# Performance work log

Measured on AMD Instinct MI355X. Metric: run time of the kernel, lower is better.

## Reference

```python
import jax, jax.numpy as jnp
import numpy as np

ND, NPR, DD, DP, LAT, AT, B = 2048, 2048, 128, 128, 128, 32, 16384


def setup_inputs():
    key = jax.random.key(0)
    ks = jax.random.split(key, 20)
    s = 0.05
    d = {}
    d["e_p_adj"] = (jax.random.uniform(ks[0], (ND, NPR)) < 0.05).astype(jnp.float32)
    d["e_e_adj"] = (jax.random.uniform(ks[1], (ND, ND)) < 0.05).astype(jnp.float32)
    d["p_p_adj"] = (jax.random.uniform(ks[2], (NPR, NPR)) < 0.05).astype(jnp.float32)
    d["input_disease"] = jax.random.randint(ks[3], (B,), 0, ND)
    d["input_drug"] = jax.random.randint(ks[4], (B,), 0, NPR)
    d["labels"] = jax.random.randint(ks[5], (B,), 0, 2)
    # learned parameters
    d["disease_emb"] = jax.random.normal(ks[6], (ND, DD)) * s
    d["drug_emb"] = jax.random.normal(ks[7], (NPR, DP)) * s
    d["Wdg"] = jax.random.normal(ks[8], (DP, LAT)) * s   # disease_gcn_w
    d["bdg_lin"] = jnp.zeros((LAT,))                      # Linear bias
    d["bdg"] = jnp.zeros((LAT,))                          # extra disease_gcn_b
    d["Wpg"] = jax.random.normal(ks[9], (DD, LAT)) * s   # drug_gcn_w
    d["bpg_lin"] = jnp.zeros((LAT,))
    d["bpg"] = jnp.zeros((LAT,))
    d["Wa1_d"] = jax.random.normal(ks[10], (DP + DD, AT)) * s  # concat [key(drug), query(disease)]
    d["ba1_d"] = jnp.zeros((AT,))
    d["Wa2_d"] = jax.random.normal(ks[11], (AT, 1)) * s
    d["ba2_d"] = jnp.zeros((1,))
    d["Wa1_p"] = jax.random.normal(ks[12], (DD + DP, AT)) * s  # concat [key(disease), query(drug)]
    d["ba1_p"] = jnp.zeros((AT,))
    d["Wa2_p"] = jax.random.normal(ks[13], (AT, 1)) * s
    d["ba2_p"] = jnp.zeros((1,))
    d["Wd2"] = jax.random.normal(ks[14], (DD, LAT)) * s  # disease_w2
    d["bd2"] = jnp.zeros((LAT,))
    d["Wp3"] = jax.random.normal(ks[15], (DP, LAT)) * s  # drug_w3
    d["bp3"] = jnp.zeros((LAT,))
    d["mlp_W1"] = jax.random.normal(ks[16], (LAT, DD)) * s
    d["mlp_b1"] = jnp.zeros((DD,))
    d["mlp_W2"] = jax.random.normal(ks[17], (DD, DD)) * s
    d["mlp_b2"] = jnp.zeros((DD,))
    d["Wpred"] = jax.random.normal(ks[18], (DD, 1)) * s
    d["bpred"] = jnp.zeros((1,))
    return d


def _attention_gcn(adj, other, selfe, W1, b1, W2, b2):
    # torch: concat([key=other, query=self]) -> Linear(W1) ; split W1 instead of
    # materializing the [Ns, No, Dk+Dq] concat tensor (same math, less HBM traffic)
    do = other.shape[1]
    ko = other @ W1[:do]              # [No, A]
    qs = selfe @ W1[do:]              # [Ns, A]
    h = jax.nn.relu(qs[:, None, :] + ko[None, :, :] + b1)   # [Ns, No, A]
    alpha = jax.nn.relu(jnp.squeeze(h @ W2, -1) + b2[0])    # [Ns, No]
    alpha = alpha * adj
    return jax.nn.softmax(alpha, axis=1) @ other            # [Ns, Do]


def _forward(e_p_adj, e_e_adj, p_p_adj, input_disease, input_drug, labels,
             disease_emb, drug_emb, Wdg, bdg_lin, bdg, Wpg, bpg_lin, bpg,
             Wa1_d, ba1_d, Wa2_d, ba2_d, Wa1_p, ba1_p, Wa2_p, ba2_p,
             Wd2, bd2, Wp3, bp3, mlp_W1, mlp_b1, mlp_W2, mlp_b2, Wpred, bpred):
    h_e_gcn = _attention_gcn(e_p_adj, drug_emb, disease_emb, Wa1_d, ba1_d, Wa2_d, ba2_d)
    h_e_gcn = h_e_gcn @ Wdg + bdg_lin + bdg
    h_p_gcn = _attention_gcn(e_p_adj.T, disease_emb, drug_emb, Wa1_p, ba1_p, Wa2_p, ba2_p)
    h_p_gcn = h_p_gcn @ Wpg + bpg_lin + bpg
    # disease knn branch
    deg_d = jnp.sum(e_e_adj, axis=1, keepdims=True) + 1e-8
    h_e_e = ((e_e_adj @ disease_emb) / deg_d) @ Wd2 + bd2
    h_e = jax.nn.selu(h_e_gcn + h_e_e)
    # drug knn branch
    deg_p = jnp.sum(p_p_adj, axis=1, keepdims=True) + 1e-8
    h_p_p = ((p_p_adj @ drug_emb) / deg_p) @ Wp3 + bp3
    h_p = jax.nn.selu(h_p_gcn + h_p_p)
    # pair prediction MLP
    x = h_e[input_disease] * h_p[input_drug]                # [B, LAT]
    x = jax.nn.selu(x @ mlp_W1 + mlp_b1)
    x = jax.nn.selu(x @ mlp_W2 + mlp_b2)
    z = jnp.squeeze(x @ Wpred, -1) + bpred[0]               # [B]
    y = labels.astype(jnp.float32)
    # BCEWithLogitsLoss (stable), mean reduction
    loss = jnp.mean(jnp.maximum(z, 0.0) - z * y + jnp.log1p(jnp.exp(-jnp.abs(z))))
    return (loss, jax.nn.sigmoid(z))


def reference(e_p_adj, e_e_adj, p_p_adj, input_disease, input_drug, labels,
              disease_emb, drug_emb, Wdg, bdg_lin, bdg, Wpg, bpg_lin, bpg,
              Wa1_d, ba1_d, Wa2_d, ba2_d, Wa1_p, ba1_p, Wa2_p, ba2_p,
              Wd2, bd2, Wp3, bp3, mlp_W1, mlp_b1, mlp_W2, mlp_b2, Wpred, bpred):
    return _forward(e_p_adj, e_e_adj, p_p_adj, input_disease, input_drug, labels,
                    disease_emb, drug_emb, Wdg, bdg_lin, bdg, Wpg, bpg_lin, bpg,
                    Wa1_d, ba1_d, Wa2_d, ba2_d, Wa1_p, ba1_p, Wa2_p, ba2_p,
                    Wd2, bd2, Wp3, bp3, mlp_W1, mlp_b1, mlp_W2, mlp_b2, Wpred, bpred)
```

## Files before the change

### kernel.cpp

```cpp
#include <hip/hip_runtime.h>

#define ND   2048
#define BB   16384

typedef unsigned short u16;
typedef unsigned int u32;
typedef __attribute__((ext_vector_type(8))) short short8;
typedef __attribute__((ext_vector_type(4))) float f32x4;

__device__ inline float bf2f(u16 u) {
    union { u32 i; float f; } v; v.i = ((u32)u) << 16; return v.f;
}
__device__ inline u16 f2bf(float f) {
    union { float f; u32 i; } v; v.f = f;
    u32 i = v.i + 0x7fffu + ((v.i >> 16) & 1u);
    return (u16)(i >> 16);
}
__device__ inline float seluf(float x) {
    const float sc = 1.0507009873554805f, al = 1.6732632423543772f;
    return x > 0.f ? sc * x : sc * al * expm1f(x);
}

__device__ inline bool sniff_f32(const void* demb_raw, void* lds) {
    int tid = threadIdx.x;
    int* redf = (int*)lds;
    const u16* p6 = (const u16*)demb_raw;
    int sane = 0;
    #pragma unroll
    for (int i = 0; i < 2; i++) {
        u16 u = p6[4 * tid + 2 * i];
        int e = (u >> 7) & 0xFF;
        if (u == 0 || (e >= 0x66 && e <= 0x8C)) sane++;
    }
    redf[tid] = sane;
    __syncthreads();
    for (int o = 128; o > 0; o >>= 1) {
        if (tid < o) redf[tid] += redf[tid + o];
        __syncthreads();
    }
    bool f32 = redf[0] < 300;
    __syncthreads();
    return f32;
}

#define NSEG 26
struct CvtArgs { const void* src[NSEG]; int off[NSEG]; int n[NSEG]; };
struct CS {
    const void* adj[3];
    u16* ridx[3]; u32* rcnt[3];
    const void* demb_raw;
    u32* cntT; float* lossacc; u32* losscnt;
};

__global__ __launch_bounds__(256) void cvtcsr(CvtArgs a, u16* __restrict__ base, CS c) {
    int bx = blockIdx.x;
    int t = threadIdx.x;
    __shared__ int sniffbuf[256];
    bool f32 = sniff_f32(c.demb_raw, sniffbuf);
    if (bx < 8) c.cntT[bx * 256 + t] = 0u;
    if (bx == 8 && t == 0) { c.lossacc[0] = 0.f; c.losscnt[0] = 0u; }
    if (bx < 1536) {
        int m = bx >> 9;
        int r0 = (bx & 511) * 4;
        int lane = t & 63;
        __shared__ u32 lcnt[4];
        if (t < 4) lcnt[t] = 0;
        __syncthreads();
        float v[4][8];
        int c0 = t * 8;
        if (f32) {
            #pragma unroll
            for (int rr = 0; rr < 4; rr++) {
                const float4* p = (const float4*)((const float*)c.adj[m] +
                                                  (size_t)(r0 + rr) * 2048 + c0);
                float4 x = p[0], y = p[1];
                v[rr][0] = x.x; v[rr][1] = x.y; v[rr][2] = x.z; v[rr][3] = x.w;
                v[rr][4] = y.x; v[rr][5] = y.y; v[rr][6] = y.z; v[rr][7] = y.w;
            }
        } else {
            #pragma unroll
            for (int rr = 0; rr < 4; rr++) {
                const uint4* p = (const uint4*)((const u16*)c.adj[m] +
                                                (size_t)(r0 + rr) * 2048 + c0);
                uint4 x = p[0];
                u32 u[4] = {x.x, x.y, x.z, x.w};
                #pragma unroll
                for (int i = 0; i < 4; i++) {
                    v[rr][2 * i + 0] = (u[i] & 0xffffu) ? 1.f : 0.f;
                    v[rr][2 * i + 1] = (u[i] >> 16)     ? 1.f : 0.f;
                }
            }
        }
        #pragma unroll
        for (int rr = 0; rr < 4; rr++) {
            int cnt = 0;
            #pragma unroll
            for (int i = 0; i < 8; i++) cnt += (v[rr][i] != 0.f) ? 1 : 0;
            int pfx = cnt;
            #pragma unroll
            for (int o = 1; o < 64; o <<= 1) {
                int s = __shfl_up(pfx, o, 64);
                if (lane >= o) pfx += s;
            }
            int wtot = __shfl(pfx, 63, 64);
            u32 wb = 0;
            if (lane == 0) wb = atomicAdd(&lcnt[rr], (u32)wtot);
            wb = __shfl((int)wb, 0, 64);
            int o = (int)wb + pfx - cnt;
            u16* ridx = c.ridx[m] + (size_t)(r0 + rr) * 2048;
            #pragma unroll
            for (int i = 0; i < 8; i++) {
                if (v[rr][i] != 0.f) ridx[o++] = (u16)(c0 + i);
            }
        }
        __syncthreads();
        if (t < 4) c.rcnt[m][r0 + t] = lcnt[t];
    } else {
        int idx = bx - 1536;
        int seg = idx >> 6, xb = idx & 63;
        int n = a.n[seg];
        const void* s = a.src[seg];
        u16* d = base + a.off[seg];
        int nw = n >> 1;
        if (f32) {
            const float2* sf = (const float2*)s;
            u32* dw = (u32*)d;
            for (int i = xb * 256 + t; i < nw; i += 16384) {
                float2 v = sf[i];
                dw[i] = (u32)f2bf(v.x) | ((u32)f2bf(v.y) << 16);
            }
        } else {
            const u32* sw = (const u32*)s;
            u32* dw = (u32*)d;
            for (int i = xb * 256 + t; i < nw; i += 16384) dw[i] = sw[i];
        }
        if ((n & 1) && xb == 0 && t == 0)
            d[n - 1] = f32 ? f2bf(((const float*)s)[n - 1]) : ((const u16*)s)[n - 1];
    }
}

struct PR {
    const u16* demb; const u16* pemb;
    const u16* Wa1d; const u16* ba1d;
    const u16* Wa1p; const u16* ba1p;
    float* ko_d; float* qs_d; float* ko_p; float* qs_p;
    const u16* idx0; const u32* cnt0; u16* cidx; u32* ccnt;
    const u16* ts[6]; u16* W1T; u16* W2T; u16* WcTe; u16* WcTp;
    const u16* ba[3]; const u16* bb[3]; u16* b_e; u16* b_p;
    float* csd; float* csp;
    const u16* avgidx[2]; const u32* avgcnt[2]; const u16* avgemb[2]; u16* avgout[2];
};

__global__ __launch_bounds__(256) void prep2(PR p) {
    int bx = blockIdx.x;
    int tid = threadIdx.x;
    __shared__ float sx[2][128];
    __shared__ float sred[2][128];
    __shared__ u16 stile[32][33];
    __shared__ float st0[256], st1[256];
    __shared__ u16 Wl[4096];

    if (bx < 4) {
        int id = bx;
        int m = id >> 1, half = id & 1;
        const u16* e = m ? p.pemb : p.demb;
        int c2 = tid & 31, rg = tid >> 5;
        int dbase = half * 64;
        float s0 = 0.f, s1 = 0.f;
        for (int it = 0; it < 256; it++) {
            int row = it * 8 + rg;
            u32 v = *(const u32*)(e + (size_t)row * 128 + dbase + c2 * 2);
            s0 += bf2f((u16)(v & 0xffffu));
            s1 += bf2f((u16)(v >> 16));
        }
        st0[tid] = s0; st1[tid] = s1;
        __syncthreads();
        if (tid < 32) {
            float a0 = 0.f, a1 = 0.f;
            #pragma unroll
            for (int g = 0; g < 8; g++) { a0 += st0[g * 32 + tid]; a1 += st1[g * 32 + tid]; }
            float* cs = m ? p.csp : p.csd;
            cs[dbase + tid * 2 + 0] = a0;
            cs[dbase + tid * 2 + 1] = a1;
        }
        if (tid < 64) {
            int d = dbase + tid;
            if (m == 0)
                p.b_e[d] = f2bf(bf2f(p.ba[0][d]) + bf2f(p.ba[1][d]) + bf2f(p.ba[2][d]));
            else
                p.b_p[d] = f2bf(bf2f(p.bb[0][d]) + bf2f(p.bb[1][d]) + bf2f(p.bb[2][d]));
        }
    } else if (bx < 2052) {
        int r = bx - 4;
        int n = (int)p.cnt0[r];
        const u16* row = p.idx0 + (size_t)r * 2048;
        for (int i = tid; i < n; i += 256) {
            int cc = (int)row[i];
            u32 q = atomicAdd(&p.ccnt[cc], 1u);
            p.cidx[(size_t)cc * 2048 + q] = (u16)r;
        }
    } else if (bx < 3076) {
        int id = bx - 2052;
        int task = id >> 9, blk = id & 511;
        int wv = tid >> 6, lane = tid & 63;
        int grp = lane >> 4, dim = lane & 15;
        int r = blk * 4 + wv;
        const u16* idx = p.avgidx[task] + (size_t)r * 2048;
        int nnz = (int)p.avgcnt[task][r];
        const u16* emb = p.avgemb[task];
        float acc[8];
        #pragma unroll
        for (int t = 0; t < 8; t++) acc[t] = 0.f;
        for (int base = 0; base < nnz; base += 64) {
            int i = base + lane;
            int j = (i < nnz) ? (int)idx[i] : 0;
            int cend = min(64, nnz - base);
            #pragma unroll 4
            for (int k4 = 0; k4 < cend; k4 += 4) {
                int kk = k4 + grp;
                int jk = __shfl(j, kk, 64);
                float wk = (base + kk < nnz) ? 1.f : 0.f;
                const uint4* pp = (const uint4*)((const char*)emb + jk * 256 + dim * 16);
                uint4 vv = *pp;
                u32 u[4] = {vv.x, vv.y, vv.z, vv.w};
                #pragma unroll
                for (int cc = 0; cc < 4; cc++) {
                    acc[2 * cc + 0] = fmaf(wk, bf2f((u16)(u[cc] & 0xffffu)), acc[2 * cc + 0]);
                    acc[2 * cc + 1] = fmaf(wk, bf2f((u16)(u[cc] >> 16)), acc[2 * cc + 1]);
                }
            }
        }
        #pragma unroll
        for (int t = 0; t < 8; t++) {
            acc[t] += __shfl_xor(acc[t], 32, 64);
            acc[t] += __shfl_xor(acc[t], 16, 64);
        }
        if (grp == 0) {
            float sc = 1.f / ((float)nnz + 1e-8f);
            float v[8];
            #pragma unroll
            for (int t = 0; t < 8; t++) v[t] = acc[t] * sc;
            uint4 pk;
            pk.x = (u32)f2bf(v[0]) | ((u32)f2bf(v[1]) << 16);
            pk.y = (u32)f2bf(v[2]) | ((u32)f2bf(v[3]) << 16);
            pk.z = (u32)f2bf(v[4]) | ((u32)f2bf(v[5]) << 16);
            pk.w = (u32)f2bf(v[6]) | ((u32)f2bf(v[7]) << 16);
            *(uint4*)(p.avgout[task] + (size_t)r * 256 + dim * 8) = pk;
        }
    } else if (bx < 4100) {
        int blk = bx - 3076;
        int m = blk >> 8;
        int r0 = (blk & 255) * 8;
        const u16* src; const u16* W; const u16* bias; float* out;
        switch (m) {
            case 0:  src = p.pemb; W = p.Wa1d;            bias = nullptr; out = p.ko_d; break;
            case 1:  src = p.demb; W = p.Wa1d + 128 * 32; bias = p.ba1d;  out = p.qs_d; break;
            case 2:  src = p.demb; W = p.Wa1p;            bias = nullptr; out = p.ko_p; break;
            default: src = p.pemb; W = p.Wa1p + 128 * 32; bias = p.ba1p;  out = p.qs_p; break;
        }
        {
            const uint4* wsrc = (const uint4*)W;
            uint4* wdst = (uint4*)Wl;
            #pragma unroll
            for (int i = 0; i < 2; i++) wdst[i * 256 + tid] = wsrc[i * 256 + tid];
        }
        __syncthreads();
        int sub = tid >> 7, t = tid & 127;
        int a = t & 31, part = t >> 5;
        #pragma unroll 1
        for (int rp = 0; rp < 4; rp++) {
            int row = r0 + rp * 2 + sub;
            sx[sub][t] = bf2f(src[(size_t)row * 128 + t]);
            __syncthreads();
            float s = 0.f;
            #pragma unroll
            for (int k = 0; k < 32; k++)
                s += sx[sub][part * 32 + k] * bf2f(Wl[(part * 32 + k) * 32 + a]);
            sred[sub][t] = s;
            __syncthreads();
            if (part == 0) {
                float tt = sred[sub][a] + sred[sub][a + 32] + sred[sub][a + 64] + sred[sub][a + 96];
                if (bias) tt += bf2f(bias[a]);
                out[(size_t)row * 32 + a] = tt;
            }
            __syncthreads();
        }
    } else {
        int id = bx - 4100;
        int z = id >> 4, rem = id & 15;
        int c0 = (rem & 3) * 32, r0 = (rem >> 2) * 32;
        const u16* in = p.ts[z];
        u16* out; int ldo, ooff;
        switch (z) {
            case 0:  out = p.W1T;  ldo = 128; ooff = 0;   break;
            case 1:  out = p.W2T;  ldo = 128; ooff = 0;   break;
            case 2:  out = p.WcTe; ldo = 256; ooff = 0;   break;
            case 3:  out = p.WcTe; ldo = 256; ooff = 128; break;
            case 4:  out = p.WcTp; ldo = 256; ooff = 0;   break;
            default: out = p.WcTp; ldo = 256; ooff = 128; break;
        }
        int tx = tid & 31, ty = tid >> 5;
        int x = c0 + tx;
        for (int i = ty; i < 32; i += 8)
            stile[i][tx] = in[(size_t)(r0 + i) * 128 + x];
        __syncthreads();
        int rr = r0 + tx;
        for (int i = ty; i < 32; i += 8)
            out[(size_t)(c0 + i) * ldo + ooff + rr] = stile[tx][i];
    }
}

struct SP {
    const u16* idx[2]; const u32* cnt[2];
    const float* ko[2]; const float* qs[2];
    const u16* w2[2]; const u16* b2[2];
    const u16* emb[2]; const float* csum[2];
    u16* out[2];
};

__global__ __launch_bounds__(256) void spagg(SP a) {
    int task = blockIdx.y;
    int tid = threadIdx.x;
    int wv = tid >> 6, lane = tid & 63;
    int grp = lane >> 4, dim = lane & 15;
    int r = blockIdx.x * 4 + wv;
    const u16* idx = a.idx[task] + (size_t)r * 2048;
    int nnz = (int)a.cnt[task][r];
    const u16* emb = a.emb[task];
    const float* ko = a.ko[task];

    float qsr[32], w2h[32];
    {
        const float4* qp = (const float4*)(a.qs[task] + (size_t)r * 32);
        #pragma unroll
        for (int i = 0; i < 8; i++) {
            float4 v = qp[i];
            qsr[4 * i + 0] = v.x; qsr[4 * i + 1] = v.y;
            qsr[4 * i + 2] = v.z; qsr[4 * i + 3] = v.w;
        }
        #pragma unroll
        for (int i = 0; i < 32; i++) w2h[i] = bf2f(a.w2[task][i]);
    }
    float b2v = bf2f(a.b2[task][0]);

    float acc[8];
    #pragma unroll
    for (int t = 0; t < 8; t++) acc[t] = 0.f;
    float wsuml = 0.f;

    for (int base = 0; base < nnz; base += 64) {
        int i = base + lane;
        float w = 0.f;
        int j = 0;
        if (i < nnz) {
            j = (int)idx[i];
            const float4* kp = (const float4*)(ko + (size_t)j * 32);
            float s = 0.f;
            #pragma unroll
            for (int q = 0; q < 8; q++) {
                float4 kv = kp[q];
                s += fmaxf(qsr[4 * q + 0] + kv.x, 0.f) * w2h[4 * q + 0];
                s += fmaxf(qsr[4 * q + 1] + kv.y, 0.f) * w2h[4 * q + 1];
                s += fmaxf(qsr[4 * q + 2] + kv.z, 0.f) * w2h[4 * q + 2];
                s += fmaxf(qsr[4 * q + 3] + kv.w, 0.f) * w2h[4 * q + 3];
            }
            w = __expf(fmaxf(s + b2v, 0.f)) - 1.f;
            wsuml += w;
        }
        int cend = min(64, nnz - base);
        #pragma unroll 4
        for (int k4 = 0; k4 < cend; k4 += 4) {
            int kk = k4 + grp;
            float wk = __shfl(w, kk, 64);
            int jk = __shfl(j, kk, 64);
            const uint4* pp = (const uint4*)((const char*)emb + jk * 256 + dim * 16);
            uint4 vv = *pp;
            u32 u[4] = {vv.x, vv.y, vv.z, vv.w};
            #pragma unroll
            for (int cc = 0; cc < 4; cc++) {
                acc[2 * cc + 0] = fmaf(wk, bf2f((u16)(u[cc] & 0xffffu)), acc[2 * cc + 0]);
                acc[2 * cc + 1] = fmaf(wk, bf2f((u16)(u[cc] >> 16)), acc[2 * cc + 1]);
            }
        }
    }

    #pragma unroll
    for (int t = 0; t < 8; t++) {
        acc[t] += __shfl_xor(acc[t], 32, 64);
        acc[t] += __shfl_xor(acc[t], 16, 64);
    }
    #pragma unroll
    for (int o = 32; o > 0; o >>= 1) wsuml += __shfl_xor(wsuml, o, 64);

    if (grp == 0) {
        float sc = 1.f / (2048.f + wsuml);
        const float* cs = a.csum[task] + dim * 8;
        float v[8];
        #pragma unroll
        for (int t = 0; t < 8; t++) v[t] = (cs[t] + acc[t]) * sc;
        uint4 pk;
        pk.x = (u32)f2bf(v[0]) | ((u32)f2bf(v[1]) << 16);
        pk.y = (u32)f2bf(v[2]) | ((u32)f2bf(v[3]) << 16);
        pk.z = (u32)f2bf(v[4]) | ((u32)f2bf(v[5]) << 16);
        pk.w = (u32)f2bf(v[6]) | ((u32)f2bf(v[7]) << 16);
        *(uint4*)(a.out[task] + (size_t)r * 256 + dim * 8) = pk;
    }
}

struct GD4 {
    const void* A[4]; const u16* BT[4]; u16* C[4];
    const u16* bias[4]; const float* rs[4];
    int lda[4], ldb[4], ldc[4], coff[4], kiters[4], act[4], araw[4], rsmode[4];
};

#define PADK 136

__global__ __launch_bounds__(256, 2) void gemmL(GD4 g) {
    __shared__ __align__(16) u16 As[16][PADK];
    __shared__ __align__(16) u16 Bs[128][PADK];
    int z = blockIdx.y;
    const void* A = g.A[z];
    const u16* BT = g.BT[z];
    int lda = g.lda[z], ldb = g.ldb[z];
    int kiters = g.kiters[z];
    int tid = threadIdx.x;
    int lane = tid & 63, wv = tid >> 6;
    int mrow = lane & 15, quad = lane >> 4;
    int m0 = blockIdx.x * 16;
    int c0 = wv * 32;
    int sr = tid >> 4, sk = (tid & 15) * 8;
    f32x4 acc0 = {0.f, 0.f, 0.f, 0.f}, acc1 = {0.f, 0.f, 0.f, 0.f};

    short8 ra, rb[8];
    auto ldstage = [&](int kb) {
        ra = *(const short8*)((const u16*)A + (size_t)(m0 + sr) * lda + kb + sk);
        const u16* bbase = BT + (size_t)sr * ldb + kb + sk;
        #pragma unroll
        for (int i = 0; i < 8; i++)
            rb[i] = *(const short8*)(bbase + (size_t)i * 16 * ldb);
    };
    auto ststage = [&]() {
        *(short8*)(&As[sr][sk]) = ra;
        #pragma unroll
        for (int i = 0; i < 8; i++)
            *(short8*)(&Bs[i * 16 + sr][sk]) = rb[i];
    };
    auto compute = [&]() {
        #pragma unroll
        for (int ks = 0; ks < 4; ks++) {
            short8 af = *(const short8*)(&As[mrow][ks * 32 + quad * 8]);
            short8 b0 = *(const short8*)(&Bs[c0 + mrow][ks * 32 + quad * 8]);
            short8 b1 = *(const short8*)(&Bs[c0 + 16 + mrow][ks * 32 + quad * 8]);
            acc0 = __builtin_amdgcn_mfma_f32_16x16x32_bf16(af, b0, acc0, 0, 0, 0);
            acc1 = __builtin_amdgcn_mfma_f32_16x16x32_bf16(af, b1, acc1, 0, 0, 0);
        }
    };

    ldstage(0);
    #pragma unroll 1
    for (int it = 0; it < kiters - 1; ++it) {
        ststage();
        __syncthreads();
        ldstage((it + 1) * 128);
        compute();
        __syncthreads();
    }
    ststage();
    __syncthreads();
    compute();

    const float* rs = g.rs[z];
    int rsmode = g.rsmode[z];
    const u16* bi = g.bias[z];
    u16* C = g.C[z];
    int ldc = g.ldc[z], coff = g.coff[z], act = g.act[z];
    int n0 = c0 + mrow, n1 = n0 + 16;
    float bv0 = bi ? bf2f(bi[n0]) : 0.f;
    float bv1 = bi ? bf2f(bi[n1]) : 0.f;
    #pragma unroll
    for (int r = 0; r < 4; r++) {
        int row = m0 + quad * 4 + r;
        float v0 = acc0[r], v1 = acc1[r];
        if (rsmode == 1) { float sc = rs[row]; v0 *= sc; v1 *= sc; }
        else if (rsmode == 2) {
            float t = 0.f;
            #pragma unroll
            for (int p = 0; p < 8; p++) t += rs[row + p * 2048];
            float sc = 1.f / t;
            v0 *= sc; v1 *= sc;
        }
        v0 += bv0; v1 += bv1;
        if (act) { v0 = seluf(v0); v1 = seluf(v1); }
        C[(size_t)row * ldc + coff + n0] = f2bf(v0);
        C[(size_t)row * ldc + coff + n1] = f2bf(v1);
    }
}

#define PADX 136
__global__ __launch_bounds__(256, 2) void mlpfused(
    const u16* __restrict__ he, const u16* __restrict__ hp,
    const int* __restrict__ di, const int* __restrict__ dr,
    const u16* __restrict__ W1T, const u16* __restrict__ b1,
    const u16* __restrict__ W2T, const u16* __restrict__ b2,
    const u16* __restrict__ wpred, const u16* __restrict__ bpred,
    const int* __restrict__ labels,
    float* __restrict__ out, float* __restrict__ lossacc,
    u32* __restrict__ losscnt) {
    __shared__ __align__(16) u16 Xs[64][PADX];
    __shared__ __align__(16) u16 Ws[128][PADX];
    __shared__ float wred[4];
    int tid = threadIdx.x;
    int lane = tid & 63, wv = tid >> 6;
    int mrow = lane & 15, quad = lane >> 4;
    int p0 = blockIdx.x * 64;

    {
        int row = tid >> 2, sub = tid & 3;
        int b = p0 + row;
        int ia = di[b], ic = dr[b];
        const uint4* pe = (const uint4*)(he + (size_t)ia * 128 + sub * 32);
        const uint4* pp = (const uint4*)(hp + (size_t)ic * 128 + sub * 32);
        #pragma unroll
        for (int q = 0; q < 4; q++) {
            uint4 ue = pe[q], up = pp[q];
            u32 eu[4] = {ue.x, ue.y, ue.z, ue.w};
            u32 pu[4] = {up.x, up.y, up.z, up.w};
            #pragma unroll
            for (int c = 0; c < 4; c++) {
                float lo = bf2f((u16)(eu[c] & 0xffffu)) * bf2f((u16)(pu[c] & 0xffffu));
                float hi = bf2f((u16)(eu[c] >> 16)) * bf2f((u16)(pu[c] >> 16));
                *(u32*)(&Xs[row][sub * 32 + q * 8 + c * 2]) =
                    (u32)f2bf(lo) | ((u32)f2bf(hi) << 16);
            }
        }
    }
    {
        int n = tid >> 1, half = tid & 1;
        const short8* src = (const short8*)(W1T + (size_t)n * 128 + half * 64);
        short8* dst = (short8*)(&Ws[n][half * 64]);
        #pragma unroll
        for (int i = 0; i < 8; i++) dst[i] = src[i];
    }
    __syncthreads();

    f32x4 acc[8];
    #pragma unroll
    for (int nt = 0; nt < 8; nt++) acc[nt] = {0.f, 0.f, 0.f, 0.f};
    #pragma unroll
    for (int ks = 0; ks < 4; ks++) {
        short8 af = *(const short8*)(&Xs[wv * 16 + mrow][ks * 32 + quad * 8]);
        #pragma unroll
        for (int nt = 0; nt < 8; nt++) {
            short8 bfv = *(const short8*)(&Ws[nt * 16 + mrow][ks * 32 + quad * 8]);
            acc[nt] = __builtin_amdgcn_mfma_f32_16x16x32_bf16(af, bfv, acc[nt], 0, 0, 0);
        }
    }
    __syncthreads();
    #pragma unroll
    for (int nt = 0; nt < 8; nt++) {
        int col = nt * 16 + mrow;
        float bv = bf2f(b1[col]);
        #pragma unroll
        for (int r = 0; r < 4; r++) {
            int row = wv * 16 + quad * 4 + r;
            Xs[row][col] = f2bf(seluf(acc[nt][r] + bv));
        }
    }
    {
        int n = tid >> 1, half = tid & 1;
        const short8* src = (const short8*)(W2T + (size_t)n * 128 + half * 64);
        short8* dst = (short8*)(&Ws[n][half * 64]);
        #pragma unroll
        for (int i = 0; i < 8; i++) dst[i] = src[i];
    }
    __syncthreads();

    #pragma unroll
    for (int nt = 0; nt < 8; nt++) acc[nt] = {0.f, 0.f, 0.f, 0.f};
    #pragma unroll
    for (int ks = 0; ks < 4; ks++) {
        short8 af = *(const short8*)(&Xs[wv * 16 + mrow][ks * 32 + quad * 8]);
        #pragma unroll
        for (int nt = 0; nt < 8; nt++) {
            short8 bfv = *(const short8*)(&Ws[nt * 16 + mrow][ks * 32 + quad * 8]);
            acc[nt] = __builtin_amdgcn_mfma_f32_16x16x32_bf16(af, bfv, acc[nt], 0, 0, 0);
        }
    }

    float zp[4] = {0.f, 0.f, 0.f, 0.f};
    #pragma unroll
    for (int nt = 0; nt < 8; nt++) {
        int col = nt * 16 + mrow;
        float bv = bf2f(b2[col]);
        float wp = bf2f(wpred[col]);
        #pragma unroll
        for (int r = 0; r < 4; r++) {
            float x2 = bf2f(f2bf(seluf(acc[nt][r] + bv)));
            zp[r] = fmaf(x2, wp, zp[r]);
        }
    }
    #pragma unroll
    for (int r = 0; r < 4; r++) {
        #pragma unroll
        for (int o = 1; o < 16; o <<= 1) zp[r] += __shfl_xor(zp[r], o, 64);
    }
    float bpv = bf2f(bpred[0]);
    float lsum = 0.f;
    #pragma unroll
    for (int r = 0; r < 4; r++) {
        int b = p0 + wv * 16 + quad * 4 + r;
        float z = zp[r] + bpv;
        float sig = 1.f / (1.f + __expf(-z));
        if (mrow == 0) out[1 + b] = sig;
        float y = (float)labels[b];
        lsum += fmaxf(z, 0.f) - z * y + log1pf(__expf(-fabsf(z)));
    }
    lsum += __shfl_xor(lsum, 16, 64);
    lsum += __shfl_xor(lsum, 32, 64);
    if (lane == 0) wred[wv] = lsum;
    __syncthreads();
    if (tid == 0) {
        float bs = wred[0] + wred[1] + wred[2] + wred[3];
        atomicAdd(lossacc, bs);
        __threadfence();
        u32 old = atomicAdd(losscnt, 1u);
        if (old == 255u) {
            float tot = atomicAdd(lossacc, 0.f);
            out[0] = tot * (1.f / 16384.f);
        }
    }
}

extern "C" void kernel_launch(void* const* d_in, const int* in_sizes, int n_in,
                              void* d_out, int out_size, void* d_ws, size_t ws_size,
                              hipStream_t stream) {
    const void* e_p_adj = d_in[0];
    const void* e_e_adj = d_in[1];
    const void* p_p_adj = d_in[2];
    const int* in_dis  = (const int*)d_in[3];
    const int* in_drug = (const int*)d_in[4];
    const int* labels  = (const int*)d_in[5];
    float* out = (float*)d_out;

    char* ws = (char*)d_ws;
    size_t off = 0;
    auto take = [&](size_t bytes) { char* p = ws + off; off = (off + bytes + 255) & ~(size_t)255; return p; };
    u16*   A_e   = (u16*)take((size_t)2048 * 256 * 2);
    u16*   A_p   = (u16*)take((size_t)2048 * 256 * 2);
    u16*   WcTe  = (u16*)take((size_t)128 * 256 * 2);
    u16*   WcTp  = (u16*)take((size_t)128 * 256 * 2);
    u16*   W1T   = (u16*)take((size_t)128 * 128 * 2);
    u16*   W2T   = (u16*)take((size_t)128 * 128 * 2);
    u16*   b_e   = (u16*)take(256);
    u16*   b_p   = (u16*)take(256);
    u16*   h_e   = (u16*)take((size_t)2048 * 128 * 2);
    u16*   h_p   = (u16*)take((size_t)2048 * 128 * 2);
    float* ko_d  = (float*)take((size_t)2048 * 32 * 4);
    float* qs_d  = (float*)take((size_t)2048 * 32 * 4);
    float* ko_p  = (float*)take((size_t)2048 * 32 * 4);
    float* qs_p  = (float*)take((size_t)2048 * 32 * 4);
    float* csd   = (float*)take(128 * 4);
    float* csp   = (float*)take(128 * 4);
    float* lossacc = (float*)take(256);
    u32*   losscnt = (u32*)((char*)lossacc + 4);
    u16*   canon = (u16*)take((size_t)700000 * 2);
    u16*   idx0  = (u16*)take((size_t)2048 * 2048 * 2);
    u16*   idx1  = (u16*)take((size_t)2048 * 2048 * 2);
    u16*   idx2  = (u16*)take((size_t)2048 * 2048 * 2);
    u16*   idx3  = (u16*)take((size_t)2048 * 2048 * 2);
    u32*   cnt0  = (u32*)take(2048 * 4);
    u32*   cnt2  = (u32*)take(2048 * 4);
    u32*   cnt3  = (u32*)take(2048 * 4);
    u32*   cntT  = (u32*)take(2048 * 4);

    const int segidx[NSEG] = {6, 7, 14, 18, 8, 22, 11, 24, 26, 28,
                              15, 16, 17, 19, 20, 21,
                              9, 10, 12, 13, 23, 25, 27, 29, 30, 31};
    const int segn[NSEG]   = {262144, 262144, 8192, 8192, 16384, 16384, 16384, 16384, 16384, 16384,
                              32, 32, 1, 32, 32, 1,
                              128, 128, 128, 128, 128, 128, 128, 128, 128, 1};
    CvtArgs ca;
    u16* cp[NSEG];
    {
        int o = 0;
        for (int i = 0; i < NSEG; i++) {
            ca.src[i] = d_in[segidx[i]];
            ca.off[i] = o;
            ca.n[i] = segn[i];
            cp[i] = canon + o;
            o += (segn[i] + 15) & ~15;
        }
    }
    u16 *cdemb = cp[0], *cpemb = cp[1], *cWa1d = cp[2], *cWa1p = cp[3];
    u16 *cWdg = cp[4], *cWd2 = cp[5], *cWpg = cp[6], *cWp3 = cp[7];
    u16 *cW1 = cp[8], *cW2 = cp[9];
    u16 *cba1d = cp[10], *cWa2d = cp[11], *cba2d = cp[12];
    u16 *cba1p = cp[13], *cWa2p = cp[14], *cba2p = cp[15];
    u16 *cbdg_lin = cp[16], *cbdg = cp[17], *cbpg_lin = cp[18], *cbpg = cp[19];
    u16 *cbd2 = cp[20], *cbp3 = cp[21], *cmb1 = cp[22], *cmb2 = cp[23];
    u16 *cWpred = cp[24], *cbpred = cp[25];

    {
        CS cs;
        cs.adj[0] = e_p_adj; cs.ridx[0] = idx0; cs.rcnt[0] = cnt0;
        cs.adj[1] = e_e_adj; cs.ridx[1] = idx2; cs.rcnt[1] = cnt2;
        cs.adj[2] = p_p_adj; cs.ridx[2] = idx3; cs.rcnt[2] = cnt3;
        cs.demb_raw = d_in[6];
        cs.cntT = cntT; cs.lossacc = lossacc; cs.losscnt = losscnt;
        cvtcsr<<<1536 + 64 * NSEG, 256, 0, stream>>>(ca, canon, cs);
    }

    PR pr;
    pr.demb = cdemb; pr.pemb = cpemb;
    pr.Wa1d = cWa1d; pr.ba1d = cba1d; pr.Wa1p = cWa1p; pr.ba1p = cba1p;
    pr.ko_d = ko_d; pr.qs_d = qs_d; pr.ko_p = ko_p; pr.qs_p = qs_p;
    pr.idx0 = idx0; pr.cnt0 = cnt0; pr.cidx = idx1; pr.ccnt = cntT;
    pr.ts[0] = cW1; pr.ts[1] = cW2; pr.ts[2] = cWdg;
    pr.ts[3] = cWd2; pr.ts[4] = cWpg; pr.ts[5] = cWp3;
    pr.W1T = W1T; pr.W2T = W2T; pr.WcTe = WcTe; pr.WcTp = WcTp;
    pr.ba[0] = cbdg_lin; pr.ba[1] = cbdg; pr.ba[2] = cbd2;
    pr.bb[0] = cbpg_lin; pr.bb[1] = cbpg; pr.bb[2] = cbp3;
    pr.b_e = b_e; pr.b_p = b_p; pr.csd = csd; pr.csp = csp;
    pr.avgidx[0] = idx2; pr.avgcnt[0] = cnt2; pr.avgemb[0] = cdemb; pr.avgout[0] = A_e + 128;
    pr.avgidx[1] = idx3; pr.avgcnt[1] = cnt3; pr.avgemb[1] = cpemb; pr.avgout[1] = A_p + 128;
    prep2<<<4196, 256, 0, stream>>>(pr);

    {
        SP sp;
        sp.idx[0] = idx0; sp.cnt[0] = cnt0; sp.ko[0] = ko_d; sp.qs[0] = qs_d;
        sp.w2[0] = cWa2d; sp.b2[0] = cba2d; sp.emb[0] = cpemb; sp.csum[0] = csp;
        sp.out[0] = A_e;
        sp.idx[1] = idx1; sp.cnt[1] = cntT; sp.ko[1] = ko_p; sp.qs[1] = qs_p;
        sp.w2[1] = cWa2p; sp.b2[1] = cba2p; sp.emb[1] = cdemb; sp.csum[1] = csd;
        sp.out[1] = A_p;
        spagg<<<dim3(512, 2), 256, 0, stream>>>(sp);
    }

    auto setd = [](GD4& g, int z, const void* A, int lda, const u16* BT, int ldb,
                   u16* C, int ldc, int coff, int ki, const u16* bi,
                   const float* rs, int act, int araw, int rm) {
        g.A[z] = A; g.lda[z] = lda; g.BT[z] = BT; g.ldb[z] = ldb;
        g.C[z] = C; g.ldc[z] = ldc; g.coff[z] = coff; g.kiters[z] = ki;
        g.bias[z] = bi; g.rs[z] = rs; g.act[z] = act; g.araw[z] = araw; g.rsmode[z] = rm;
    };

    {
        GD4 g;
        setd(g, 0, A_e, 256, WcTe, 256, h_e, 128, 0, 2, b_e, nullptr, 1, 0, 0);
        setd(g, 1, A_p, 256, WcTp, 256, h_p, 128, 0, 2, b_p, nullptr, 1, 0, 0);
        setd(g, 2, A_e, 256, WcTe, 256, h_e, 128, 0, 2, b_e, nullptr, 1, 0, 0);
        setd(g, 3, A_e, 256, WcTe, 256, h_e, 128, 0, 2, b_e, nullptr, 1, 0, 0);
        gemmL<<<dim3(128, 2), 256, 0, stream>>>(g);
    }

    mlpfused<<<256, 256, 0, stream>>>(h_e, h_p, in_dis, in_drug,
                                      W1T, cmb1, W2T, cmb2,
                                      cWpred, cbpred, labels, out,
                                      lossacc, losscnt);
}
```

Baseline: 225.2 us.

## Fuse sparse aggregation, neighbor averaging and GCN GEMM into one kernel

Moves the neighbor-average step out of the prep kernel and merges it with the attention-weighted sparse aggregation and the per-row 256x128 projection plus SELU into a single kernel, spaggemm. Each block builds its 4 concatenated rows in shared memory and multiplies them by the transposed weights with scalar FMAs. This drops the A_e/A_p intermediate buffers and two kernel launches. In exchange, the MFMA-based gemmL is replaced by scalar bf16 dot products that read weight rows from global memory for every block, and the averaging work now runs serially after the attention aggregation inside each wave.

```diff
diff --git a/kernel.cpp b/kernel.cpp
--- a/kernel.cpp
+++ b/kernel.cpp
@@ -148,7 +148,6 @@
     const u16* ts[6]; u16* W1T; u16* W2T; u16* WcTe; u16* WcTp;
     const u16* ba[3]; const u16* bb[3]; u16* b_e; u16* b_p;
     float* csd; float* csp;
-    const u16* avgidx[2]; const u32* avgcnt[2]; const u16* avgemb[2]; u16* avgout[2];
 };
 
 __global__ __launch_bounds__(256) void prep2(PR p) {
@@ -200,14 +199,171 @@
             p.cidx[(size_t)cc * 2048 + q] = (u16)r;
         }
     } else if (bx < 3076) {
-        int id = bx - 2052;
-        int task = id >> 9, blk = id & 511;
-        int wv = tid >> 6, lane = tid & 63;
-        int grp = lane >> 4, dim = lane & 15;
-        int r = blk * 4 + wv;
-        const u16* idx = p.avgidx[task] + (size_t)r * 2048;
-        int nnz = (int)p.avgcnt[task][r];
-        const u16* emb = p.avgemb[task];
+        int blk = bx - 2052;
+        int m = blk >> 8;
+        int r0 = (blk & 255) * 8;
+        const u16* src; const u16* W; const u16* bias; float* out;
+        switch (m) {
+            case 0:  src = p.pemb; W = p.Wa1d;            bias = nullptr; out = p.ko_d; break;
+            case 1:  src = p.demb; W = p.Wa1d + 128 * 32; bias = p.ba1d;  out = p.qs_d; break;
+            case 2:  src = p.demb; W = p.Wa1p;            bias = nullptr; out = p.ko_p; break;
+            default: src = p.pemb; W = p.Wa1p + 128 * 32; bias = p.ba1p;  out = p.qs_p; break;
+        }
+        {
+            const uint4* wsrc = (const uint4*)W;
+            uint4* wdst = (uint4*)Wl;
+            #pragma unroll
+            for (int i = 0; i < 2; i++) wdst[i * 256 + tid] = wsrc[i * 256 + tid];
+        }
+        __syncthreads();
+        int sub = tid >> 7, t = tid & 127;
+        int a = t & 31, part = t >> 5;
+        #pragma unroll 1
+        for (int rp = 0; rp < 4; rp++) {
+            int row = r0 + rp * 2 + sub;
+            sx[sub][t] = bf2f(src[(size_t)row * 128 + t]);
+            __syncthreads();
+            float s = 0.f;
+            #pragma unroll
+            for (int k = 0; k < 32; k++)
+                s += sx[sub][part * 32 + k] * bf2f(Wl[(part * 32 + k) * 32 + a]);
+            sred[sub][t] = s;
+            __syncthreads();
+            if (part == 0) {
+                float tt = sred[sub][a] + sred[sub][a + 32] + sred[sub][a + 64] + sred[sub][a + 96];
+                if (bias) tt += bf2f(bias[a]);
+                out[(size_t)row * 32 + a] = tt;
+            }
+            __syncthreads();
+        }
+    } else {
+        int id = bx - 3076;
+        int z = id >> 4, rem = id & 15;
+        int c0 = (rem & 3) * 32, r0 = (rem >> 2) * 32;
+        const u16* in = p.ts[z];
+        u16* out; int ldo, ooff;
+        switch (z) {
+            case 0:  out = p.W1T;  ldo = 128; ooff = 0;   break;
+            case 1:  out = p.W2T;  ldo = 128; ooff = 0;   break;
+            case 2:  out = p.WcTe; ldo = 256; ooff = 0;   break;
+            case 3:  out = p.WcTe; ldo = 256; ooff = 128; break;
+            case 4:  out = p.WcTp; ldo = 256; ooff = 0;   break;
+            default: out = p.WcTp; ldo = 256; ooff = 128; break;
+        }
+        int tx = tid & 31, ty = tid >> 5;
+        int x = c0 + tx;
+        for (int i = ty; i < 32; i += 8)
+            stile[i][tx] = in[(size_t)(r0 + i) * 128 + x];
+        __syncthreads();
+        int rr = r0 + tx;
+        for (int i = ty; i < 32; i += 8)
+            out[(size_t)(c0 + i) * ldo + ooff + rr] = stile[tx][i];
+    }
+}
+
+struct SG {
+    const u16* aidx[2]; const u32* acnt[2];
+    const float* ko[2]; const float* qs[2];
+    const u16* w2[2]; const u16* b2[2];
+    const u16* aemb[2]; const float* csum[2];
+    const u16* vidx[2]; const u32* vcnt[2]; const u16* vemb[2];
+    const u16* WT[2]; const u16* bias[2]; u16* H[2];
+};
+
+__global__ __launch_bounds__(256) void spaggemm(SG a) {
+    int side = blockIdx.y;
+    int tid = threadIdx.x;
+    int wv = tid >> 6, lane = tid & 63;
+    int grp = lane >> 4, dim = lane & 15;
+    int r = blockIdx.x * 4 + wv;
+    __shared__ __align__(16) u16 Arow[4][256];
+
+    {
+        const u16* idx = a.aidx[side] + (size_t)r * 2048;
+        int nnz = (int)a.acnt[side][r];
+        const u16* emb = a.aemb[side];
+        const float* ko = a.ko[side];
+        float qsr[32], w2h[32];
+        {
+            const float4* qp = (const float4*)(a.qs[side] + (size_t)r * 32);
+            #pragma unroll
+            for (int i = 0; i < 8; i++) {
+                float4 v = qp[i];
+                qsr[4 * i + 0] = v.x; qsr[4 * i + 1] = v.y;
+                qsr[4 * i + 2] = v.z; qsr[4 * i + 3] = v.w;
+            }
+            #pragma unroll
+            for (int i = 0; i < 32; i++) w2h[i] = bf2f(a.w2[side][i]);
+        }
+        float b2v = bf2f(a.b2[side][0]);
+
+        float acc[8];
+        #pragma unroll
+        for (int t = 0; t < 8; t++) acc[t] = 0.f;
+        float wsuml = 0.f;
+
+        for (int base = 0; base < nnz; base += 64) {
+            int i = base + lane;
+            float w = 0.f;
+            int j = 0;
+            if (i < nnz) {
+                j = (int)idx[i];
+                const float4* kp = (const float4*)(ko + (size_t)j * 32);
+                float s = 0.f;
+                #pragma unroll
+                for (int q = 0; q < 8; q++) {
+                    float4 kv = kp[q];
+                    s += fmaxf(qsr[4 * q + 0] + kv.x, 0.f) * w2h[4 * q + 0];
+                    s += fmaxf(qsr[4 * q + 1] + kv.y, 0.f) * w2h[4 * q + 1];
+                    s += fmaxf(qsr[4 * q + 2] + kv.z, 0.f) * w2h[4 * q + 2];
+                    s += fmaxf(qsr[4 * q + 3] + kv.w, 0.f) * w2h[4 * q + 3];
+                }
+                w = __expf(fmaxf(s + b2v, 0.f)) - 1.f;
+                wsuml += w;
+            }
+            int cend = min(64, nnz - base);
+            #pragma unroll 4
+            for (int k4 = 0; k4 < cend; k4 += 4) {
+                int kk = k4 + grp;
+                float wk = __shfl(w, kk, 64);
+                int jk = __shfl(j, kk, 64);
+                const uint4* pp = (const uint4*)((const char*)emb + jk * 256 + dim * 16);
+                uint4 vv = *pp;
+                u32 u[4] = {vv.x, vv.y, vv.z, vv.w};
+                #pragma unroll
+                for (int cc = 0; cc < 4; cc++) {
+                    acc[2 * cc + 0] = fmaf(wk, bf2f((u16)(u[cc] & 0xffffu)), acc[2 * cc + 0]);
+                    acc[2 * cc + 1] = fmaf(wk, bf2f((u16)(u[cc] >> 16)), acc[2 * cc + 1]);
+                }
+            }
+        }
+        #pragma unroll
+        for (int t = 0; t < 8; t++) {
+            acc[t] += __shfl_xor(acc[t], 32, 64);
+            acc[t] += __shfl_xor(acc[t], 16, 64);
+        }
+        #pragma unroll
+        for (int o = 32; o > 0; o >>= 1) wsuml += __shfl_xor(wsuml, o, 64);
+
+        if (grp == 0) {
+            float sc = 1.f / (2048.f + wsuml);
+            const float* cs = a.csum[side] + dim * 8;
+            float v[8];
+            #pragma unroll
+            for (int t = 0; t < 8; t++) v[t] = (cs[t] + acc[t]) * sc;
+            uint4 pk;
+            pk.x = (u32)f2bf(v[0]) | ((u32)f2bf(v[1]) << 16);
+            pk.y = (u32)f2bf(v[2]) | ((u32)f2bf(v[3]) << 16);
+            pk.z = (u32)f2bf(v[4]) | ((u32)f2bf(v[5]) << 16);
+            pk.w = (u32)f2bf(v[6]) | ((u32)f2bf(v[7]) << 16);
+            *(uint4*)(&Arow[wv][dim * 8]) = pk;
+        }
+    }
+
+    {
+        const u16* idx = a.vidx[side] + (size_t)r * 2048;
+        int nnz = (int)a.vcnt[side][r];
+        const u16* emb = a.vemb[side];
         float acc[8];
         #pragma unroll
         for (int t = 0; t < 8; t++) acc[t] = 0.f;
@@ -245,254 +401,33 @@
             pk.y = (u32)f2bf(v[2]) | ((u32)f2bf(v[3]) << 16);
             pk.z = (u32)f2bf(v[4]) | ((u32)f2bf(v[5]) << 16);
             pk.w = (u32)f2bf(v[6]) | ((u32)f2bf(v[7]) << 16);
-            *(uint4*)(p.avgout[task] + (size_t)r * 256 + dim * 8) = pk;
-        }
-    } else if (bx < 4100) {
-        int blk = bx - 3076;
-        int m = blk >> 8;
-        int r0 = (blk & 255) * 8;
-        const u16* src; const u16* W; const u16* bias; float* out;
-        switch (m) {
-            case 0:  src = p.pemb; W = p.Wa1d;            bias = nullptr; out = p.ko_d; break;
-            case 1:  src = p.demb; W = p.Wa1d + 128 * 32; bias = p.ba1d;  out = p.qs_d; break;
-            case 2:  src = p.demb; W = p.Wa1p;            bias = nullptr; out = p.ko_p; break;
-            default: src = p.pemb; W = p.Wa1p + 128 * 32; bias = p.ba1p;  out = p.qs_p; break;
-        }
-        {
-            const uint4* wsrc = (const uint4*)W;
-            uint4* wdst = (uint4*)Wl;
-            #pragma unroll
-            for (int i = 0; i < 2; i++) wdst[i * 256 + tid] = wsrc[i * 256 + tid];
-        }
-        __syncthreads();
-        int sub = tid >> 7, t = tid & 127;
-        int a = t & 31, part = t >> 5;
-        #pragma unroll 1
-        for (int rp = 0; rp < 4; rp++) {
-            int row = r0 + rp * 2 + sub;
-            sx[sub][t] = bf2f(src[(size_t)row * 128 + t]);
-            __syncthreads();
-            float s = 0.f;
-            #pragma unroll
-            for (int k = 0; k < 32; k++)
-                s += sx[sub][part * 32 + k] * bf2f(Wl[(part * 32 + k) * 32 + a]);
-            sred[sub][t] = s;
-            __syncthreads();
-            if (part == 0) {
-                float tt = sred[sub][a] + sred[sub][a + 32] + sred[sub][a + 64] + sred[sub][a + 96];
-                if (bias) tt += bf2f(bias[a]);
-                out[(size_t)row * 32 + a] = tt;
-            }
-            __syncthreads();
-        }
-    } else {
-        int id = bx - 4100;
-        int z = id >> 4, rem = id & 15;
-        int c0 = (rem & 3) * 32, r0 = (rem >> 2) * 32;
-        const u16* in = p.ts[z];
-        u16* out; int ldo, ooff;
-        switch (z) {
-            case 0:  out = p.W1T;  ldo = 128; ooff = 0;   break;
-            case 1:  out = p.W2T;  ldo = 128; ooff = 0;   break;
-            case 2:  out = p.WcTe; ldo = 256; ooff = 0;   break;
-            case 3:  out = p.WcTe; ldo = 256; ooff = 128; break;
-            case 4:  out = p.WcTp; ldo = 256; ooff = 0;   break;
-            default: out = p.WcTp; ldo = 256; ooff = 128; break;
-        }
-        int tx = tid & 31, ty = tid >> 5;
-        int x = c0 + tx;
-        for (int i = ty; i < 32; i += 8)
-            stile[i][tx] = in[(size_t)(r0 + i) * 128 + x];
-        __syncthreads();
-        int rr = r0 + tx;
-        for (int i = ty; i < 32; i += 8)
-            out[(size_t)(c0 + i) * ldo + ooff + rr] = stile[tx][i];
-    }
-}
-
-struct SP {
-    const u16* idx[2]; const u32* cnt[2];
-    const float* ko[2]; const float* qs[2];
-    const u16* w2[2]; const u16* b2[2];
-    const u16* emb[2]; const float* csum[2];
-    u16* out[2];
-};
-
-__global__ __launch_bounds__(256) void spagg(SP a) {
-    int task = blockIdx.y;
-    int tid = threadIdx.x;
-    int wv = tid >> 6, lane = tid & 63;
-    int grp = lane >> 4, dim = lane & 15;
-    int r = blockIdx.x * 4 + wv;
-    const u16* idx = a.idx[task] + (size_t)r * 2048;
-    int nnz = (int)a.cnt[task][r];
-    const u16* emb = a.emb[task];
-    const float* ko = a.ko[task];
-
-    float qsr[32], w2h[32];
-    {
-        const float4* qp = (const float4*)(a.qs[task] + (size_t)r * 32);
-        #pragma unroll
-        for (int i = 0; i < 8; i++) {
-            float4 v = qp[i];
-            qsr[4 * i + 0] = v.x; qsr[4 * i + 1] = v.y;
-            qsr[4 * i + 2] = v.z; qsr[4 * i + 3] = v.w;
-        }
-        #pragma unroll
-        for (int i = 0; i < 32; i++) w2h[i] = bf2f(a.w2[task][i]);
-    }
-    float b2v = bf2f(a.b2[task][0]);
-
-    float acc[8];
-    #pragma unroll
-    for (int t = 0; t < 8; t++) acc[t] = 0.f;
-    float wsuml = 0.f;
-
-    for (int base = 0; base < nnz; base += 64) {
-        int i = base + lane;
-        float w = 0.f;
-        int j = 0;
-        if (i < nnz) {
-            j = (int)idx[i];
-            const float4* kp = (const float4*)(ko + (size_t)j * 32);
-            float s = 0.f;
-            #pragma unroll
-            for (int q = 0; q < 8; q++) {
-                float4 kv = kp[q];
-                s += fmaxf(qsr[4 * q + 0] + kv.x, 0.f) * w2h[4 * q + 0];
-                s += fmaxf(qsr[4 * q + 1] + kv.y, 0.f) * w2h[4 * q + 1];
-                s += fmaxf(qsr[4 * q + 2] + kv.z, 0.f) * w2h[4 * q + 2];
-                s += fmaxf(qsr[4 * q + 3] + kv.w, 0.f) * w2h[4 * q + 3];
-            }
-            w = __expf(fmaxf(s + b2v, 0.f)) - 1.f;
-            wsuml += w;
-        }
-        int cend = min(64, nnz - base);
-        #pragma unroll 4
-        for (int k4 = 0; k4 < cend; k4 += 4) {
-            int kk = k4 + grp;
-            float wk = __shfl(w, kk, 64);
-            int jk = __shfl(j, kk, 64);
-            const uint4* pp = (const uint4*)((const char*)emb + jk * 256 + dim * 16);
-            uint4 vv = *pp;
-            u32 u[4] = {vv.x, vv.y, vv.z, vv.w};
-            #pragma unroll
-            for (int cc = 0; cc < 4; cc++) {
-                acc[2 * cc + 0] = fmaf(wk, bf2f((u16)(u[cc] & 0xffffu)), acc[2 * cc + 0]);
-                acc[2 * cc + 1] = fmaf(wk, bf2f((u16)(u[cc] >> 16)), acc[2 * cc + 1]);
-            }
-        }
-    }
-
-    #pragma unroll
-    for (int t = 0; t < 8; t++) {
-        acc[t] += __shfl_xor(acc[t], 32, 64);
-        acc[t] += __shfl_xor(acc[t], 16, 64);
-    }
-    #pragma unroll
-    for (int o = 32; o > 0; o >>= 1) wsuml += __shfl_xor(wsuml, o, 64);
-
-    if (grp == 0) {
-        float sc = 1.f / (2048.f + wsuml);
-        const float* cs = a.csum[task] + dim * 8;
-        float v[8];
-        #pragma unroll
-        for (int t = 0; t < 8; t++) v[t] = (cs[t] + acc[t]) * sc;
-        uint4 pk;
-        pk.x = (u32)f2bf(v[0]) | ((u32)f2bf(v[1]) << 16);
-        pk.y = (u32)f2bf(v[2]) | ((u32)f2bf(v[3]) << 16);
-        pk.z = (u32)f2bf(v[4]) | ((u32)f2bf(v[5]) << 16);
-        pk.w = (u32)f2bf(v[6]) | ((u32)f2bf(v[7]) << 16);
-        *(uint4*)(a.out[task] + (size_t)r * 256 + dim * 8) = pk;
-    }
-}
-
-struct GD4 {
-    const void* A[4]; const u16* BT[4]; u16* C[4];
-    const u16* bias[4]; const float* rs[4];
-    int lda[4], ldb[4], ldc[4], coff[4], kiters[4], act[4], araw[4], rsmode[4];
-};
-
-#define PADK 136
-
-__global__ __launch_bounds__(256, 2) void gemmL(GD4 g) {
-    __shared__ __align__(16) u16 As[16][PADK];
-    __shared__ __align__(16) u16 Bs[128][PADK];
-    int z = blockIdx.y;
-    const void* A = g.A[z];
-    const u16* BT = g.BT[z];
-    int lda = g.lda[z], ldb = g.ldb[z];
-    int kiters = g.kiters[z];
-    int tid = threadIdx.x;
-    int lane = tid & 63, wv = tid >> 6;
-    int mrow = lane & 15, quad = lane >> 4;
-    int m0 = blockIdx.x * 16;
-    int c0 = wv * 32;
-    int sr = tid >> 4, sk = (tid & 15) * 8;
-    f32x4 acc0 = {0.f, 0.f, 0.f, 0.f}, acc1 = {0.f, 0.f, 0.f, 0.f};
-
-    short8 ra, rb[8];
-    auto ldstage = [&](int kb) {
-        ra = *(const short8*)((const u16*)A + (size_t)(m0 + sr) * lda + kb + sk);
-        const u16* bbase = BT + (size_t)sr * ldb + kb + sk;
-        #pragma unroll
-        for (int i = 0; i < 8; i++)
-            rb[i] = *(const short8*)(bbase + (size_t)i * 16 * ldb);
-    };
-    auto ststage = [&]() {
-        *(short8*)(&As[sr][sk]) = ra;
-        #pragma unroll
-        for (int i = 0; i < 8; i++)
-            *(short8*)(&Bs[i * 16 + sr][sk]) = rb[i];
-    };
-    auto compute = [&]() {
-        #pragma unroll
-        for (int ks = 0; ks < 4; ks++) {
-            short8 af = *(const short8*)(&As[mrow][ks * 32 + quad * 8]);
-            short8 b0 = *(const short8*)(&Bs[c0 + mrow][ks * 32 + quad * 8]);
-            short8 b1 = *(const short8*)(&Bs[c0 + 16 + mrow][ks * 32 + quad * 8]);
-            acc0 = __builtin_amdgcn_mfma_f32_16x16x32_bf16(af, b0, acc0, 0, 0, 0);
-            acc1 = __builtin_amdgcn_mfma_f32_16x16x32_bf16(af, b1, acc1, 0, 0, 0);
-        }
-    };
-
-    ldstage(0);
-    #pragma unroll 1
-    for (int it = 0; it < kiters - 1; ++it) {
-        ststage();
-        __syncthreads();
-        ldstage((it + 1) * 128);
-        compute();
-        __syncthreads();
-    }
-    ststage();
+            *(uint4*)(&Arow[wv][128 + dim * 8]) = pk;
+        }
+    }
     __syncthreads();
-    compute();
-
-    const float* rs = g.rs[z];
-    int rsmode = g.rsmode[z];
-    const u16* bi = g.bias[z];
-    u16* C = g.C[z];
-    int ldc = g.ldc[z], coff = g.coff[z], act = g.act[z];
-    int n0 = c0 + mrow, n1 = n0 + 16;
-    float bv0 = bi ? bf2f(bi[n0]) : 0.f;
-    float bv1 = bi ? bf2f(bi[n1]) : 0.f;
-    #pragma unroll
-    for (int r = 0; r < 4; r++) {
-        int row = m0 + quad * 4 + r;
-        float v0 = acc0[r], v1 = acc1[r];
-        if (rsmode == 1) { float sc = rs[row]; v0 *= sc; v1 *= sc; }
-        else if (rsmode == 2) {
-            float t = 0.f;
-            #pragma unroll
-            for (int p = 0; p < 8; p++) t += rs[row + p * 2048];
-            float sc = 1.f / t;
-            v0 *= sc; v1 *= sc;
-        }
-        v0 += bv0; v1 += bv1;
-        if (act) { v0 = seluf(v0); v1 = seluf(v1); }
-        C[(size_t)row * ldc + coff + n0] = f2bf(v0);
-        C[(size_t)row * ldc + coff + n1] = f2bf(v1);
+
+    {
+        const u16* WT = a.WT[side];
+        const u16* bi = a.bias[side];
+        u16* H = a.H[side];
+        int n = tid & 127;
+        int rh = tid >> 7;
+        float bv = bf2f(bi[n]);
+        const u32* w32 = (const u32*)(WT + (size_t)n * 256);
+        #pragma unroll
+        for (int p = 0; p < 2; p++) {
+            int row = p * 2 + rh;
+            const u32* a32 = (const u32*)(&Arow[row][0]);
+            float acc = 0.f;
+            #pragma unroll 8
+            for (int k2 = 0; k2 < 128; k2++) {
+                u32 av = a32[k2], wvv = w32[k2];
+                acc = fmaf(bf2f((u16)(av & 0xffffu)), bf2f((u16)(wvv & 0xffffu)), acc);
+                acc = fmaf(bf2f((u16)(av >> 16)), bf2f((u16)(wvv >> 16)), acc);
+            }
+            float h = seluf(acc + bv);
+            H[(size_t)(blockIdx.x * 4 + row) * 128 + n] = f2bf(h);
+        }
     }
 }
 
@@ -527,7 +462,7 @@
             u32 pu[4] = {up.x, up.y, up.z, up.w};
             #pragma unroll
             for (int c = 0; c < 4; c++) {
-                float lo = bf2f((u16)(eu[c] & 0xffffu)) * bf2f((u16)(pu[c] & 0xffffu));
+                float lo = bf2f((u16)(eu[c] & 0xffff)) * bf2f((u16)(pu[c] & 0xffff));
                 float hi = bf2f((u16)(eu[c] >> 16)) * bf2f((u16)(pu[c] >> 16));
                 *(u32*)(&Xs[row][sub * 32 + q * 8 + c * 2]) =
                     (u32)f2bf(lo) | ((u32)f2bf(hi) << 16);
@@ -645,8 +580,6 @@
     char* ws = (char*)d_ws;
     size_t off = 0;
     auto take = [&](size_t bytes) { char* p = ws + off; off = (off + bytes + 255) & ~(size_t)255; return p; };
-    u16*   A_e   = (u16*)take((size_t)2048 * 256 * 2);
-    u16*   A_p   = (u16*)take((size_t)2048 * 256 * 2);
     u16*   WcTe  = (u16*)take((size_t)128 * 256 * 2);
     u16*   WcTp  = (u16*)take((size_t)128 * 256 * 2);
     u16*   W1T   = (u16*)take((size_t)128 * 128 * 2);
@@ -721,36 +654,19 @@
     pr.ba[0] = cbdg_lin; pr.ba[1] = cbdg; pr.ba[2] = cbd2;
     pr.bb[0] = cbpg_lin; pr.bb[1] = cbpg; pr.bb[2] = cbp3;
     pr.b_e = b_e; pr.b_p = b_p; pr.csd = csd; pr.csp = csp;
-    pr.avgidx[0] = idx2; pr.avgcnt[0] = cnt2; pr.avgemb[0] = cdemb; pr.avgout[0] = A_e + 128;
-    pr.avgidx[1] = idx3; pr.avgcnt[1] = cnt3; pr.avgemb[1] = cpemb; pr.avgout[1] = A_p + 128;
-    prep2<<<4196, 256, 0, stream>>>(pr);
-
-    {
-        SP sp;
-        sp.idx[0] = idx0; sp.cnt[0] = cnt0; sp.ko[0] = ko_d; sp.qs[0] = qs_d;
-        sp.w2[0] = cWa2d; sp.b2[0] = cba2d; sp.emb[0] = cpemb; sp.csum[0] = csp;
-        sp.out[0] = A_e;
-        sp.idx[1] = idx1; sp.cnt[1] = cntT; sp.ko[1] = ko_p; sp.qs[1] = qs_p;
-        sp.w2[1] = cWa2p; sp.b2[1] = cba2p; sp.emb[1] = cdemb; sp.csum[1] = csd;
-        sp.out[1] = A_p;
-        spagg<<<dim3(512, 2), 256, 0, stream>>>(sp);
-    }
-
-    auto setd = [](GD4& g, int z, const void* A, int lda, const u16* BT, int ldb,
-                   u16* C, int ldc, int coff, int ki, const u16* bi,
-                   const float* rs, int act, int araw, int rm) {
-        g.A[z] = A; g.lda[z] = lda; g.BT[z] = BT; g.ldb[z] = ldb;
-        g.C[z] = C; g.ldc[z] = ldc; g.coff[z] = coff; g.kiters[z] = ki;
-        g.bias[z] = bi; g.rs[z] = rs; g.act[z] = act; g.araw[z] = araw; g.rsmode[z] = rm;
-    };
-
-    {
-        GD4 g;
-        setd(g, 0, A_e, 256, WcTe, 256, h_e, 128, 0, 2, b_e, nullptr, 1, 0, 0);
-        setd(g, 1, A_p, 256, WcTp, 256, h_p, 128, 0, 2, b_p, nullptr, 1, 0, 0);
-        setd(g, 2, A_e, 256, WcTe, 256, h_e, 128, 0, 2, b_e, nullptr, 1, 0, 0);
-        setd(g, 3, A_e, 256, WcTe, 256, h_e, 128, 0, 2, b_e, nullptr, 1, 0, 0);
-        gemmL<<<dim3(128, 2), 256, 0, stream>>>(g);
+    prep2<<<3172, 256, 0, stream>>>(pr);
+
+    {
+        SG sg;
+        sg.aidx[0] = idx0; sg.acnt[0] = cnt0; sg.ko[0] = ko_d; sg.qs[0] = qs_d;
+        sg.w2[0] = cWa2d; sg.b2[0] = cba2d; sg.aemb[0] = cpemb; sg.csum[0] = csp;
+        sg.vidx[0] = idx2; sg.vcnt[0] = cnt2; sg.vemb[0] = cdemb;
+        sg.WT[0] = WcTe; sg.bias[0] = b_e; sg.H[0] = h_e;
+        sg.aidx[1] = idx1; sg.acnt[1] = cntT; sg.ko[1] = ko_p; sg.qs[1] = qs_p;
+        sg.w2[1] = cWa2p; sg.b2[1] = cba2p; sg.aemb[1] = cdemb; sg.csum[1] = csd;
+        sg.vidx[1] = idx3; sg.vcnt[1] = cnt3; sg.vemb[1] = cpemb;
+        sg.WT[1] = WcTp; sg.bias[1] = b_p; sg.H[1] = h_p;
+        spaggemm<<<dim3(512, 2), 256, 0, stream>>>(sg);
     }
 
     mlpfused<<<256, 256, 0, stream>>>(h_e, h_p, in_dis, in_drug,
```

New measurement: 270.5 us. 1.2x slower.
